# Kernel tuning notes

Hardware: AMD Instinct MI355X
Metric: run time of the kernel (lower is better)

Reference implementation:

```python
import jax, jax.numpy as jnp
import numpy as np

B, N, E, R, D, L = 2, 40000, 400000, 64, 64, 6
LN_EPS = 1e-5


def _layer_norm(x, g, b):
    mu = jnp.mean(x, axis=-1, keepdims=True)
    var = jnp.var(x, axis=-1, keepdims=True)
    return (x - mu) * jax.lax.rsqrt(var + LN_EPS) * g + b


def setup_inputs() -> dict:
    key = jax.random.key(0)
    ks = jax.random.split(key, 10)
    s = 0.05
    return {
        "rel_reps": jax.random.normal(ks[0], (B, R, D), jnp.float32),
        "h_index": jax.random.randint(ks[1], (B,), 0, N, jnp.int32),
        "r_index": jax.random.randint(ks[2], (B,), 0, R, jnp.int32),
        "edge_index": jax.random.randint(ks[3], (2, E), 0, N, jnp.int32),
        "edge_type": jax.random.randint(ks[4], (E,), 0, R, jnp.int32),
        "proj_w1": jax.random.normal(ks[5], (L, D, D), jnp.float32) * s,
        "proj_b1": jnp.zeros((L, D), jnp.float32),
        "proj_w2": jax.random.normal(ks[6], (L, D, D), jnp.float32) * s,
        "proj_b2": jnp.zeros((L, D), jnp.float32),
        "lin_w": jax.random.normal(ks[7], (L, 2 * D, D), jnp.float32) * s,
        "lin_b": jnp.zeros((L, D), jnp.float32),
        "ln_g": jnp.ones((L, D), jnp.float32),
        "ln_b": jnp.zeros((L, D), jnp.float32),
        "mlp_w": jax.random.normal(ks[8], (2 * D, 2 * D), jnp.float32) * s,
        "mlp_b": jnp.zeros((2 * D,), jnp.float32),
        "num_nodes": N,
    }


def reference(rel_reps, h_index, r_index, edge_index, edge_type,
              proj_w1, proj_b1, proj_w2, proj_b2,
              lin_w, lin_b, ln_g, ln_b, mlp_w, mlp_b, num_nodes):
    # EntityNBFNet.bellmanford with 6 GeneralizedRelationalConv layers
    # (distmult message, sum aggregate, layer_norm, relu, short_cut).
    batch = rel_reps.shape[0]
    query = rel_reps[jnp.arange(batch), r_index]                     # [B, D]
    boundary = jnp.zeros((batch, num_nodes, rel_reps.shape[-1]), rel_reps.dtype)
    boundary = boundary.at[jnp.arange(batch), h_index].set(query)    # [B, N, D]
    src, dst = edge_index[0], edge_index[1]

    def layer_step(x, params):
        pw1, pb1, pw2, pb2, lw, lb, lng, lnb = params
        # per-layer relation projection MLP (project_relations=True)
        rel = jax.nn.relu(jnp.einsum("brd,de->bre", rel_reps, pw1) + pb1)
        rel = jnp.einsum("brd,de->bre", rel, pw2) + pb2              # [B, R, D]
        # distmult message: x_src * rel_edge  -> [B, E, D]
        msg = jnp.take(x, src, axis=1) * jnp.take(rel, edge_type, axis=1)
        # sum aggregation (edge_weight = ones) + boundary self-message
        agg = jax.vmap(lambda m: jax.ops.segment_sum(m, dst, num_segments=num_nodes))(msg)
        agg = agg + boundary
        out = jnp.concatenate([x, agg], axis=-1) @ lw + lb           # [B, N, D]
        out = jax.nn.relu(_layer_norm(out, lng, lnb))
        out = out + x                                                # short cut
        return out, None

    x, _ = jax.lax.scan(layer_step, boundary,
                        (proj_w1, proj_b1, proj_w2, proj_b2, lin_w, lin_b, ln_g, ln_b))
    node_query = jnp.broadcast_to(query[:, None, :], x.shape)        # [B, N, D]
    feature = jnp.concatenate([x, node_query], axis=-1)              # [B, N, 2D]
    # embedd_out=True: MLP = Linear(2D, 2D) + ReLU
    embedd = jax.nn.relu(feature @ mlp_w + mlp_b)
    return embedd
```

## Files before the change

kernel.cpp:

```cpp
#include <hip/hip_runtime.h>
#include <hip/hip_bf16.h>

namespace {

constexpr int B = 2;
constexpr int N = 40000;
constexpr int E = 400000;
constexpr int R = 64;
constexpr int D = 64;
constexpr int L = 6;
constexpr float EPS = 1e-5f;
constexpr int NB = (N + 255) / 256;
constexpr int EB = (E + 255) / 256;

typedef _Float16 v8h __attribute__((ext_vector_type(8)));
typedef _Float16 v2h __attribute__((ext_vector_type(2)));
typedef float    v4f __attribute__((ext_vector_type(4)));

__device__ __forceinline__ unsigned int pack_h2(float a, float b) {
  v2h p; p.x = (_Float16)a; p.y = (_Float16)b;
  return __builtin_bit_cast(unsigned int, p);
}
__device__ __forceinline__ float2 unpack_h2(unsigned int u) {
  v2h p = __builtin_bit_cast(v2h, u);
  return make_float2((float)p.x, (float)p.y);
}


__global__ void k_init(const float* __restrict__ rel_reps,
                       const int* __restrict__ h_index, const int* __restrict__ r_index,
                       unsigned int* __restrict__ xb,
                       _Float16* __restrict__ xrow0, _Float16* __restrict__ xrow1,
                       float* __restrict__ query_f, _Float16* __restrict__ qh) {
  int d = threadIdx.x;
  int h0 = h_index[0], h1 = h_index[1];
  float q0 = rel_reps[r_index[0] * D + d];
  float q1 = rel_reps[(R + r_index[1]) * D + d];
  query_f[d * 2] = q0; query_f[d * 2 + 1] = q1;
  qh[d]     = (_Float16)q0;
  qh[D + d] = (_Float16)q1;
  if (h0 == h1) {
    xb[(size_t)h0 * D + d] = pack_h2(q0, q1);
  } else {
    xb[(size_t)h0 * D + d] = pack_h2(q0, 0.f);
    xb[(size_t)h1 * D + d] = pack_h2(0.f, q1);
  }
  xrow0[(size_t)h0 * 2 * D + d] = (_Float16)q0;
  xrow1[(size_t)h1 * 2 * D + d] = (_Float16)q1;
}

__global__ __launch_bounds__(64) void k_rel(
    const float* __restrict__ rel_reps,
    const float* __restrict__ pw1, const float* __restrict__ pb1,
    const float* __restrict__ pw2, const float* __restrict__ pb2,
    float* __restrict__ rel_f) {
  __shared__ float row[D];
  __shared__ float row2[D];
  int idx = blockIdx.x;
  int l = idx / (B * R);
  int br = idx - l * (B * R);
  int b = br / R, r = br - b * R;
  int d = threadIdx.x;
  row[d] = rel_reps[(size_t)br * D + d];
  __syncthreads();
  const float* w1 = pw1 + (size_t)l * D * D;
  float acc = pb1[l * D + d];
  for (int k = 0; k < D; ++k) acc = fmaf(row[k], w1[k * D + d], acc);
  row2[d] = fmaxf(acc, 0.f);
  __syncthreads();
  const float* w2 = pw2 + (size_t)l * D * D;
  float acc2 = pb2[l * D + d];
  for (int k = 0; k < D; ++k) acc2 = fmaf(row2[k], w2[k * D + d], acc2);
  rel_f[(((size_t)l * R + r) * D + d) * 2 + b] = acc2;
}

__global__ __launch_bounds__(256) void k_pack_rel(const float2* __restrict__ rel2,
                                                  unsigned int* __restrict__ rel_pk) {
  int i = blockIdx.x * 256 + threadIdx.x;
  if (i < L * R * D) {
    float2 v = rel2[i];
    rel_pk[i] = pack_h2(v.x, v.y);
  }
}

__global__ __launch_bounds__(64) void k_pack_w(const float* __restrict__ lin_w,
                                               unsigned short* __restrict__ Wf) {
  int idx = blockIdx.x;
  int l = idx >> 4;
  int ct = (idx >> 2) & 3, ks = idx & 3;
  int lane = threadIdx.x;
  int n = ct * 16 + (lane & 15);
  #pragma unroll
  for (int j = 0; j < 8; ++j) {
    int k = ks * 32 + (lane >> 4) * 8 + j;
    _Float16 v = (_Float16)lin_w[(size_t)l * 2 * D * D + (size_t)k * D + n];
    Wf[(size_t)l * 8192 + ((size_t)(ct * 4 + ks) * 64 + lane) * 8 + j] =
        __builtin_bit_cast(unsigned short, v);
  }
}

__global__ __launch_bounds__(64) void k_pack_wm(const float* __restrict__ mlp_w,
                                                unsigned short* __restrict__ Wm) {
  int idx = blockIdx.x;
  int ct = idx >> 2, ks = idx & 3;
  int lane = threadIdx.x;
  int n = ct * 16 + (lane & 15);
  #pragma unroll
  for (int j = 0; j < 8; ++j) {
    int k = ks * 32 + (lane >> 4) * 8 + j;
    _Float16 v = (_Float16)mlp_w[(size_t)k * 2 * D + n];
    Wm[((size_t)idx * 64 + lane) * 8 + j] = __builtin_bit_cast(unsigned short, v);
  }
}

__global__ __launch_bounds__(256) void k_hist(const int* __restrict__ dst,
                                              int* __restrict__ cnt) {
  int e = blockIdx.x * 256 + threadIdx.x;
  if (e < E) atomicAdd(&cnt[dst[e]], 1);
}

__global__ __launch_bounds__(256) void k_scan1(const int* __restrict__ cnt,
                                               int* __restrict__ row_ptr,
                                               int* __restrict__ bsum) {
  __shared__ int s[256];
  int t = threadIdx.x;
  int i = blockIdx.x * 256 + t;
  int v = (i < N) ? cnt[i] : 0;
  s[t] = v;
  __syncthreads();
  #pragma unroll
  for (int off = 1; off < 256; off <<= 1) {
    int u = (t >= off) ? s[t - off] : 0;
    __syncthreads();
    s[t] += u;
    __syncthreads();
  }
  if (i < N) row_ptr[i] = s[t] - v;
  if (t == 255) bsum[blockIdx.x] = s[255];
}

__global__ __launch_bounds__(256) void k_scan2(int* __restrict__ bsum,
                                               int* __restrict__ row_ptr) {
  __shared__ int s[NB];
  int t = threadIdx.x;
  if (t < NB) s[t] = bsum[t];
  __syncthreads();
  if (t == 0) {
    int run = 0;
    for (int i = 0; i < NB; ++i) { int v = s[i]; s[i] = run; run += v; }
    row_ptr[N] = run;
  }
  __syncthreads();
  if (t < NB) bsum[t] = s[t];
}

__global__ __launch_bounds__(256) void k_scan3(int* __restrict__ row_ptr,
                                               const int* __restrict__ bsum,
                                               int* __restrict__ cursor) {
  int i = blockIdx.x * 256 + threadIdx.x;
  if (i < N) {
    int v = row_ptr[i] + bsum[blockIdx.x];
    row_ptr[i] = v;
    cursor[i] = v;
  }
}

__global__ __launch_bounds__(256) void k_fill(const int* __restrict__ src,
                                              const int* __restrict__ dst,
                                              const int* __restrict__ etype,
                                              int* __restrict__ cursor,
                                              unsigned int* __restrict__ es) {
  int e = blockIdx.x * 256 + threadIdx.x;
  if (e < E) {
    int p = atomicAdd(&cursor[dst[e]], 1);
    es[p] = (unsigned int)src[e] | ((unsigned int)etype[e] << 16);
  }
}

__global__ __launch_bounds__(256, 8) void k_gather(
    const unsigned int* __restrict__ xb,
    _Float16* __restrict__ xrow0, _Float16* __restrict__ xrow1,
    const unsigned int* __restrict__ rel_pk,
    const int* __restrict__ row_ptr, const unsigned int* __restrict__ es,
    const float2* __restrict__ q2, const int* __restrict__ h_index, int first) {
  int tid = threadIdx.x;
  int lane = tid & 63;
  int n = (blockIdx.x * 256 + tid) >> 6;
  int h0 = h_index[0], h1 = h_index[1];
  int rs = row_ptr[n], re = row_ptr[n + 1];
  int m = min(re - rs, 64);
  unsigned int pkl = 0;
  if (lane < m) pkl = es[rs + lane];
  float a0 = 0.f, a1 = 0.f;
  if (first) {
    for (int j = 0; j < m; ++j) {
      unsigned int pk = __shfl(pkl, j);
      int s  = (int)(pk & 0xffffu);
      int et = (int)(pk >> 16);
      if (s == h0) { float2 xf = unpack_h2(xb[(size_t)s * D + lane]);
                     float2 rf = unpack_h2(rel_pk[et * D + lane]);
                     a0 = fmaf(xf.x, rf.x, a0); }
      if (s == h1) { float2 xf = unpack_h2(xb[(size_t)s * D + lane]);
                     float2 rf = unpack_h2(rel_pk[et * D + lane]);
                     a1 = fmaf(xf.y, rf.y, a1); }
    }
    for (int jj = rs + 64; jj < re; ++jj) {
      unsigned int pk = es[jj];
      int s  = (int)(pk & 0xffffu);
      int et = (int)(pk >> 16);
      if (s == h0) { float2 xf = unpack_h2(xb[(size_t)s * D + lane]);
                     float2 rf = unpack_h2(rel_pk[et * D + lane]);
                     a0 = fmaf(xf.x, rf.x, a0); }
      if (s == h1) { float2 xf = unpack_h2(xb[(size_t)s * D + lane]);
                     float2 rf = unpack_h2(rel_pk[et * D + lane]);
                     a1 = fmaf(xf.y, rf.y, a1); }
    }
  } else {
    int j = 0;
    for (; j + 4 <= m; j += 4) {
      unsigned int p0 = __shfl(pkl, j),     p1 = __shfl(pkl, j + 1);
      unsigned int p2 = __shfl(pkl, j + 2), p3 = __shfl(pkl, j + 3);
      unsigned int xa  = xb[(size_t)(p0 & 0xffffu) * D + lane];
      unsigned int xbv = xb[(size_t)(p1 & 0xffffu) * D + lane];
      unsigned int xc  = xb[(size_t)(p2 & 0xffffu) * D + lane];
      unsigned int xd  = xb[(size_t)(p3 & 0xffffu) * D + lane];
      unsigned int ra = rel_pk[(p0 >> 16) * D + lane];
      unsigned int rb = rel_pk[(p1 >> 16) * D + lane];
      unsigned int rc = rel_pk[(p2 >> 16) * D + lane];
      unsigned int rd = rel_pk[(p3 >> 16) * D + lane];
      float2 xf, rf;
      xf = unpack_h2(xa);  rf = unpack_h2(ra);
      a0 = fmaf(xf.x, rf.x, a0); a1 = fmaf(xf.y, rf.y, a1);
      xf = unpack_h2(xbv); rf = unpack_h2(rb);
      a0 = fmaf(xf.x, rf.x, a0); a1 = fmaf(xf.y, rf.y, a1);
      xf = unpack_h2(xc);  rf = unpack_h2(rc);
      a0 = fmaf(xf.x, rf.x, a0); a1 = fmaf(xf.y, rf.y, a1);
      xf = unpack_h2(xd);  rf = unpack_h2(rd);
      a0 = fmaf(xf.x, rf.x, a0); a1 = fmaf(xf.y, rf.y, a1);
    }
    for (; j < m; ++j) {
      unsigned int pk = __shfl(pkl, j);
      float2 xf = unpack_h2(xb[(size_t)(pk & 0xffffu) * D + lane]);
      float2 rf = unpack_h2(rel_pk[(pk >> 16) * D + lane]);
      a0 = fmaf(xf.x, rf.x, a0); a1 = fmaf(xf.y, rf.y, a1);
    }
    for (int jj = rs + 64; jj < re; ++jj) {
      unsigned int pk = es[jj];
      float2 xf = unpack_h2(xb[(size_t)(pk & 0xffffu) * D + lane]);
      float2 rf = unpack_h2(rel_pk[(pk >> 16) * D + lane]);
      a0 = fmaf(xf.x, rf.x, a0); a1 = fmaf(xf.y, rf.y, a1);
    }
  }
  if (n == h0) a0 += q2[lane].x;
  if (n == h1) a1 += q2[lane].y;
  xrow0[(size_t)n * 2 * D + D + lane] = (_Float16)a0;
  xrow1[(size_t)n * 2 * D + D + lane] = (_Float16)a1;
}

__global__ __launch_bounds__(64) void k_linear(
    unsigned int* __restrict__ xb,
    _Float16* __restrict__ xrow0, _Float16* __restrict__ xrow1,
    const unsigned short* __restrict__ Wf,
    const float* __restrict__ lin_b, const float* __restrict__ ln_g,
    const float* __restrict__ ln_b, int layer) {
  int lane = threadIdx.x;
  int nb = blockIdx.x * 16;
  int c = lane & 15, rg = lane >> 4;
  const v8h* wf = (const v8h*)(Wf + (size_t)layer * 8192);
  v8h Bf[4][4];
  #pragma unroll
  for (int ct = 0; ct < 4; ++ct)
    #pragma unroll
    for (int ks = 0; ks < 4; ++ks)
      Bf[ct][ks] = wf[(ct * 4 + ks) * 64 + lane];
  v4f acc0[4], acc1[4];
  #pragma unroll
  for (int ct = 0; ct < 4; ++ct) {
    acc0[ct] = (v4f){0.f, 0.f, 0.f, 0.f};
    acc1[ct] = (v4f){0.f, 0.f, 0.f, 0.f};
  }
  #pragma unroll
  for (int ks = 0; ks < 4; ++ks) {
    size_t aoff = (size_t)(nb + c) * 2 * D + ks * 32 + rg * 8;
    v8h A0 = *(const v8h*)(xrow0 + aoff);
    v8h A1 = *(const v8h*)(xrow1 + aoff);
    #pragma unroll
    for (int ct = 0; ct < 4; ++ct) {
      acc0[ct] = __builtin_amdgcn_mfma_f32_16x16x32_f16(A0, Bf[ct][ks], acc0[ct], 0, 0, 0);
      acc1[ct] = __builtin_amdgcn_mfma_f32_16x16x32_f16(A1, Bf[ct][ks], acc1[ct], 0, 0, 0);
    }
  }
  float bias4[4], g4[4], be4[4];
  #pragma unroll
  for (int ct = 0; ct < 4; ++ct) {
    int d = ct * 16 + c;
    bias4[ct] = lin_b[layer * D + d];
    g4[ct]    = ln_g[layer * D + d];
    be4[ct]   = ln_b[layer * D + d];
  }
  #pragma unroll
  for (int j = 0; j < 4; ++j) {
    int node = nb + rg * 4 + j;
    float v0[4], v1[4];
    float s10 = 0.f, s20 = 0.f, s11 = 0.f, s21 = 0.f;
    #pragma unroll
    for (int ct = 0; ct < 4; ++ct) {
      v0[ct] = acc0[ct][j] + bias4[ct];
      v1[ct] = acc1[ct][j] + bias4[ct];
      s10 += v0[ct]; s20 += v0[ct] * v0[ct];
      s11 += v1[ct]; s21 += v1[ct] * v1[ct];
    }
    #pragma unroll
    for (int mk = 1; mk < 16; mk <<= 1) {
      s10 += __shfl_xor(s10, mk); s20 += __shfl_xor(s20, mk);
      s11 += __shfl_xor(s11, mk); s21 += __shfl_xor(s21, mk);
    }
    float mu0 = s10 * (1.f / D), var0 = s20 * (1.f / D) - mu0 * mu0;
    float mu1 = s11 * (1.f / D), var1 = s21 * (1.f / D) - mu1 * mu1;
    float rs0 = rsqrtf(var0 + EPS), rs1 = rsqrtf(var1 + EPS);
    #pragma unroll
    for (int ct = 0; ct < 4; ++ct) {
      int d = ct * 16 + c;
      float o0 = fmaxf((v0[ct] - mu0) * rs0 * g4[ct] + be4[ct], 0.f);
      float o1 = fmaxf((v1[ct] - mu1) * rs1 * g4[ct] + be4[ct], 0.f);
      float2 xv = unpack_h2(xb[(size_t)node * D + d]);
      float r0 = o0 + xv.x, r1 = o1 + xv.y;
      xb[(size_t)node * D + d] = pack_h2(r0, r1);
      xrow0[(size_t)node * 2 * D + d] = (_Float16)r0;
      xrow1[(size_t)node * 2 * D + d] = (_Float16)r1;
    }
  }
}

__global__ __launch_bounds__(64) void k_mlp(
    const _Float16* __restrict__ xrow0, const _Float16* __restrict__ xrow1,
    const _Float16* __restrict__ qh,
    const unsigned short* __restrict__ Wm,
    const float* __restrict__ mlp_b,
    float* __restrict__ outf) {
  int lane = threadIdx.x;
  int nb = blockIdx.x * 16;
  int c = lane & 15, rg = lane >> 4;
  const v8h* wm = (const v8h*)Wm;
  v4f acc0[8], acc1[8];
  #pragma unroll
  for (int ct = 0; ct < 8; ++ct) {
    acc0[ct] = (v4f){0.f, 0.f, 0.f, 0.f};
    acc1[ct] = (v4f){0.f, 0.f, 0.f, 0.f};
  }
  #pragma unroll
  for (int ks = 0; ks < 4; ++ks) {
    v8h A0, A1;
    if (ks < 2) {
      size_t aoff = (size_t)(nb + c) * 2 * D + ks * 32 + rg * 8;
      A0 = *(const v8h*)(xrow0 + aoff);
      A1 = *(const v8h*)(xrow1 + aoff);
    } else {
      int qoff = (ks - 2) * 32 + rg * 8;
      A0 = *(const v8h*)(qh + qoff);
      A1 = *(const v8h*)(qh + D + qoff);
    }
    #pragma unroll
    for (int ct = 0; ct < 8; ++ct) {
      v8h Bv = wm[(ct * 4 + ks) * 64 + lane];
      acc0[ct] = __builtin_amdgcn_mfma_f32_16x16x32_f16(A0, Bv, acc0[ct], 0, 0, 0);
      acc1[ct] = __builtin_amdgcn_mfma_f32_16x16x32_f16(A1, Bv, acc1[ct], 0, 0, 0);
    }
  }
  #pragma unroll
  for (int ct = 0; ct < 8; ++ct) {
    int d = ct * 16 + c;
    float bias = mlp_b[d];
    #pragma unroll
    for (int j = 0; j < 4; ++j) {
      int node = nb + rg * 4 + j;
      outf[(size_t)node * 2 * D + d]       = fmaxf(acc0[ct][j] + bias, 0.f);
      outf[((size_t)N + node) * 2 * D + d] = fmaxf(acc1[ct][j] + bias, 0.f);
    }
  }
}

}

extern "C" void kernel_launch(void* const* d_in, const int* in_sizes, int n_in,
                              void* d_out, int out_size, void* d_ws, size_t ws_size,
                              hipStream_t stream) {
  const float* rel_reps = (const float*)d_in[0];
  const int* h_index    = (const int*)d_in[1];
  const int* r_index    = (const int*)d_in[2];
  const int* edge_index = (const int*)d_in[3];
  const int* edge_type  = (const int*)d_in[4];
  const float* proj_w1  = (const float*)d_in[5];
  const float* proj_b1  = (const float*)d_in[6];
  const float* proj_w2  = (const float*)d_in[7];
  const float* proj_b2  = (const float*)d_in[8];
  const float* lin_w    = (const float*)d_in[9];
  const float* lin_b    = (const float*)d_in[10];
  const float* ln_g     = (const float*)d_in[11];
  const float* ln_b     = (const float*)d_in[12];
  const float* mlp_w    = (const float*)d_in[13];
  const float* mlp_b    = (const float*)d_in[14];

  float* rel_all = (float*)d_ws;
  float* query   = rel_all + (size_t)2 * L * R * D;
  int*   cnt     = (int*)(query + 2 * D);
  int*   row_ptr = cnt + N;
  int*   cursor  = row_ptr + (N + 1);
  unsigned int* es  = (unsigned int*)(cursor + N);
  int*   bsum    = (int*)(es + E);
  unsigned int* xb = (unsigned int*)(bsum + NB);
  unsigned int* rel_pk = xb + (size_t)N * D;
  unsigned short* Wf = (unsigned short*)(rel_pk + (size_t)L * R * D);
  _Float16* xrow0 = (_Float16*)(Wf + (size_t)L * 8192);
  _Float16* xrow1 = xrow0 + (size_t)N * 2 * D;
  unsigned short* Wm = (unsigned short*)(xrow1 + (size_t)N * 2 * D);
  _Float16* qh = (_Float16*)(Wm + 16384);

  const int* srcp = edge_index;
  const int* dstp = edge_index + E;

  hipMemsetAsync(xb, 0, (size_t)N * D * sizeof(unsigned int), stream);
  hipMemsetAsync(xrow0, 0, (size_t)N * 2 * D * sizeof(_Float16) * 2, stream);
  hipMemsetAsync(cnt, 0, N * sizeof(int), stream);
  k_init<<<1, 64, 0, stream>>>(rel_reps, h_index, r_index,
                               xb, xrow0, xrow1, query, qh);
  k_rel<<<L * B * R, 64, 0, stream>>>(rel_reps, proj_w1, proj_b1, proj_w2, proj_b2, rel_all);
  k_pack_rel<<<(L * R * D + 255) / 256, 256, 0, stream>>>((const float2*)rel_all, rel_pk);
  k_pack_w<<<L * 16, 64, 0, stream>>>(lin_w, Wf);
  k_pack_wm<<<32, 64, 0, stream>>>(mlp_w, Wm);
  k_hist<<<EB, 256, 0, stream>>>(dstp, cnt);
  k_scan1<<<NB, 256, 0, stream>>>(cnt, row_ptr, bsum);
  k_scan2<<<1, 256, 0, stream>>>(bsum, row_ptr);
  k_scan3<<<NB, 256, 0, stream>>>(row_ptr, bsum, cursor);
  k_fill<<<EB, 256, 0, stream>>>(srcp, dstp, edge_type, cursor, es);

  for (int l = 0; l < L; ++l) {
    k_gather<<<N / 4, 256, 0, stream>>>(xb, xrow0, xrow1,
                                        rel_pk + (size_t)l * R * D,
                                        row_ptr, es, (const float2*)query, h_index,
                                        (l == 0) ? 1 : 0);
    k_linear<<<N / 16, 64, 0, stream>>>(xb, xrow0, xrow1,
                                        Wf, lin_b, ln_g, ln_b, l);
  }
  k_mlp<<<N / 16, 64, 0, stream>>>(xrow0, xrow1, qh, Wm, mlp_b, (float*)d_out);
}
```

Measured before the change: 393.5 us.

## Process two destination nodes per wavefront in gather with 8-byte loads

The gather kernel now splits each 64-lane wavefront into two 32-lane halves, each handling its own destination node and loading two packed feature pairs per lane with 8-byte loads. This halves the grid and is meant to raise memory-level parallelism and cut wasted lanes for low-degree nodes, since the average in-degree is about 10. In exchange the two halves run in lockstep up to the larger degree of the pair, and the neighbour buffer shrinks from 64 to 32 entries, so more edges take the slower serial tail loop.

```diff
diff --git a/kernel.cpp b/kernel.cpp
--- a/kernel.cpp
+++ b/kernel.cpp
@@ -185,76 +185,111 @@
     const float2* __restrict__ q2, const int* __restrict__ h_index, int first) {
   int tid = threadIdx.x;
   int lane = tid & 63;
-  int n = (blockIdx.x * 256 + tid) >> 6;
+  int h = lane >> 5;
+  int ln = lane & 31;
+  int w = (blockIdx.x * 256 + tid) >> 6;
+  int n = w * 2 + h;
   int h0 = h_index[0], h1 = h_index[1];
-  int rs = row_ptr[n], re = row_ptr[n + 1];
-  int m = min(re - rs, 64);
-  unsigned int pkl = 0;
-  if (lane < m) pkl = es[rs + lane];
-  float a0 = 0.f, a1 = 0.f;
+  int rp = 0;
+  if (lane < 3) rp = row_ptr[2 * w + lane];
+  int rs = __shfl(rp, h);
+  int re = __shfl(rp, h + 1);
+  int deg = re - rs;
+  int dc = min(deg, 32);
+  unsigned int esv = 0;
+  if (ln < dc) esv = es[rs + ln];
+  float a0x = 0.f, a0y = 0.f, a1x = 0.f, a1y = 0.f;
   if (first) {
-    for (int j = 0; j < m; ++j) {
-      unsigned int pk = __shfl(pkl, j);
-      int s  = (int)(pk & 0xffffu);
-      int et = (int)(pk >> 16);
-      if (s == h0) { float2 xf = unpack_h2(xb[(size_t)s * D + lane]);
-                     float2 rf = unpack_h2(rel_pk[et * D + lane]);
-                     a0 = fmaf(xf.x, rf.x, a0); }
-      if (s == h1) { float2 xf = unpack_h2(xb[(size_t)s * D + lane]);
-                     float2 rf = unpack_h2(rel_pk[et * D + lane]);
-                     a1 = fmaf(xf.y, rf.y, a1); }
-    }
-    for (int jj = rs + 64; jj < re; ++jj) {
-      unsigned int pk = es[jj];
-      int s  = (int)(pk & 0xffffu);
-      int et = (int)(pk >> 16);
-      if (s == h0) { float2 xf = unpack_h2(xb[(size_t)s * D + lane]);
-                     float2 rf = unpack_h2(rel_pk[et * D + lane]);
-                     a0 = fmaf(xf.x, rf.x, a0); }
-      if (s == h1) { float2 xf = unpack_h2(xb[(size_t)s * D + lane]);
-                     float2 rf = unpack_h2(rel_pk[et * D + lane]);
-                     a1 = fmaf(xf.y, rf.y, a1); }
+    for (int j = 0; j < dc; ++j) {
+      unsigned int pk = __shfl(esv, (h << 5) | j);
+      int s = (int)(pk & 0xffffu), et = (int)(pk >> 16);
+      if (s == h0 || s == h1) {
+        uint2 xv = *(const uint2*)&xb[(size_t)s * D + 2 * ln];
+        uint2 rv = *(const uint2*)&rel_pk[et * D + 2 * ln];
+        float2 xfx = unpack_h2(xv.x), xfy = unpack_h2(xv.y);
+        float2 rfx = unpack_h2(rv.x), rfy = unpack_h2(rv.y);
+        if (s == h0) { a0x = fmaf(xfx.x, rfx.x, a0x); a0y = fmaf(xfy.x, rfy.x, a0y); }
+        if (s == h1) { a1x = fmaf(xfx.y, rfx.y, a1x); a1y = fmaf(xfy.y, rfy.y, a1y); }
+      }
+    }
+    for (int j = rs + 32; j < re; ++j) {
+      unsigned int pk = es[j];
+      int s = (int)(pk & 0xffffu), et = (int)(pk >> 16);
+      if (s == h0 || s == h1) {
+        uint2 xv = *(const uint2*)&xb[(size_t)s * D + 2 * ln];
+        uint2 rv = *(const uint2*)&rel_pk[et * D + 2 * ln];
+        float2 xfx = unpack_h2(xv.x), xfy = unpack_h2(xv.y);
+        float2 rfx = unpack_h2(rv.x), rfy = unpack_h2(rv.y);
+        if (s == h0) { a0x = fmaf(xfx.x, rfx.x, a0x); a0y = fmaf(xfy.x, rfy.x, a0y); }
+        if (s == h1) { a1x = fmaf(xfx.y, rfx.y, a1x); a1y = fmaf(xfy.y, rfy.y, a1y); }
+      }
     }
   } else {
-    int j = 0;
-    for (; j + 4 <= m; j += 4) {
-      unsigned int p0 = __shfl(pkl, j),     p1 = __shfl(pkl, j + 1);
-      unsigned int p2 = __shfl(pkl, j + 2), p3 = __shfl(pkl, j + 3);
-      unsigned int xa  = xb[(size_t)(p0 & 0xffffu) * D + lane];
-      unsigned int xbv = xb[(size_t)(p1 & 0xffffu) * D + lane];
-      unsigned int xc  = xb[(size_t)(p2 & 0xffffu) * D + lane];
-      unsigned int xd  = xb[(size_t)(p3 & 0xffffu) * D + lane];
-      unsigned int ra = rel_pk[(p0 >> 16) * D + lane];
-      unsigned int rb = rel_pk[(p1 >> 16) * D + lane];
-      unsigned int rc = rel_pk[(p2 >> 16) * D + lane];
-      unsigned int rd = rel_pk[(p3 >> 16) * D + lane];
-      float2 xf, rf;
-      xf = unpack_h2(xa);  rf = unpack_h2(ra);
-      a0 = fmaf(xf.x, rf.x, a0); a1 = fmaf(xf.y, rf.y, a1);
-      xf = unpack_h2(xbv); rf = unpack_h2(rb);
-      a0 = fmaf(xf.x, rf.x, a0); a1 = fmaf(xf.y, rf.y, a1);
-      xf = unpack_h2(xc);  rf = unpack_h2(rc);
-      a0 = fmaf(xf.x, rf.x, a0); a1 = fmaf(xf.y, rf.y, a1);
-      xf = unpack_h2(xd);  rf = unpack_h2(rd);
-      a0 = fmaf(xf.x, rf.x, a0); a1 = fmaf(xf.y, rf.y, a1);
-    }
-    for (; j < m; ++j) {
-      unsigned int pk = __shfl(pkl, j);
-      float2 xf = unpack_h2(xb[(size_t)(pk & 0xffffu) * D + lane]);
-      float2 rf = unpack_h2(rel_pk[(pk >> 16) * D + lane]);
-      a0 = fmaf(xf.x, rf.x, a0); a1 = fmaf(xf.y, rf.y, a1);
-    }
-    for (int jj = rs + 64; jj < re; ++jj) {
-      unsigned int pk = es[jj];
-      float2 xf = unpack_h2(xb[(size_t)(pk & 0xffffu) * D + lane]);
-      float2 rf = unpack_h2(rel_pk[(pk >> 16) * D + lane]);
-      a0 = fmaf(xf.x, rf.x, a0); a1 = fmaf(xf.y, rf.y, a1);
-    }
-  }
-  if (n == h0) a0 += q2[lane].x;
-  if (n == h1) a1 += q2[lane].y;
-  xrow0[(size_t)n * 2 * D + D + lane] = (_Float16)a0;
-  xrow1[(size_t)n * 2 * D + D + lane] = (_Float16)a1;
+    int rounds = (dc + 3) >> 2;
+    int maxr = max(__shfl(rounds, 0), __shfl(rounds, 32));
+    for (int jr = 0; jr < maxr; ++jr) {
+      int j = jr * 4;
+      int i0 = max(min(j + 0, dc - 1), 0), i1 = max(min(j + 1, dc - 1), 0);
+      int i2 = max(min(j + 2, dc - 1), 0), i3 = max(min(j + 3, dc - 1), 0);
+      unsigned int p0 = __shfl(esv, (h << 5) | i0);
+      unsigned int p1 = __shfl(esv, (h << 5) | i1);
+      unsigned int p2 = __shfl(esv, (h << 5) | i2);
+      unsigned int p3 = __shfl(esv, (h << 5) | i3);
+      uint2 xv0 = *(const uint2*)&xb[(size_t)(p0 & 0xffffu) * D + 2 * ln];
+      uint2 xv1 = *(const uint2*)&xb[(size_t)(p1 & 0xffffu) * D + 2 * ln];
+      uint2 xv2 = *(const uint2*)&xb[(size_t)(p2 & 0xffffu) * D + 2 * ln];
+      uint2 xv3 = *(const uint2*)&xb[(size_t)(p3 & 0xffffu) * D + 2 * ln];
+      uint2 rv0 = *(const uint2*)&rel_pk[(p0 >> 16) * D + 2 * ln];
+      uint2 rv1 = *(const uint2*)&rel_pk[(p1 >> 16) * D + 2 * ln];
+      uint2 rv2 = *(const uint2*)&rel_pk[(p2 >> 16) * D + 2 * ln];
+      uint2 rv3 = *(const uint2*)&rel_pk[(p3 >> 16) * D + 2 * ln];
+      if (j + 0 < dc) {
+        float2 xfx = unpack_h2(xv0.x), xfy = unpack_h2(xv0.y);
+        float2 rfx = unpack_h2(rv0.x), rfy = unpack_h2(rv0.y);
+        a0x = fmaf(xfx.x, rfx.x, a0x); a1x = fmaf(xfx.y, rfx.y, a1x);
+        a0y = fmaf(xfy.x, rfy.x, a0y); a1y = fmaf(xfy.y, rfy.y, a1y);
+      }
+      if (j + 1 < dc) {
+        float2 xfx = unpack_h2(xv1.x), xfy = unpack_h2(xv1.y);
+        float2 rfx = unpack_h2(rv1.x), rfy = unpack_h2(rv1.y);
+        a0x = fmaf(xfx.x, rfx.x, a0x); a1x = fmaf(xfx.y, rfx.y, a1x);
+        a0y = fmaf(xfy.x, rfy.x, a0y); a1y = fmaf(xfy.y, rfy.y, a1y);
+      }
+      if (j + 2 < dc) {
+        float2 xfx = unpack_h2(xv2.x), xfy = unpack_h2(xv2.y);
+        float2 rfx = unpack_h2(rv2.x), rfy = unpack_h2(rv2.y);
+        a0x = fmaf(xfx.x, rfx.x, a0x); a1x = fmaf(xfx.y, rfx.y, a1x);
+        a0y = fmaf(xfy.x, rfy.x, a0y); a1y = fmaf(xfy.y, rfy.y, a1y);
+      }
+      if (j + 3 < dc) {
+        float2 xfx = unpack_h2(xv3.x), xfy = unpack_h2(xv3.y);
+        float2 rfx = unpack_h2(rv3.x), rfy = unpack_h2(rv3.y);
+        a0x = fmaf(xfx.x, rfx.x, a0x); a1x = fmaf(xfx.y, rfx.y, a1x);
+        a0y = fmaf(xfy.x, rfy.x, a0y); a1y = fmaf(xfy.y, rfy.y, a1y);
+      }
+    }
+    for (int j = rs + 32; j < re; ++j) {
+      unsigned int pk = es[j];
+      uint2 xv = *(const uint2*)&xb[(size_t)(pk & 0xffffu) * D + 2 * ln];
+      uint2 rv = *(const uint2*)&rel_pk[(pk >> 16) * D + 2 * ln];
+      float2 xfx = unpack_h2(xv.x), xfy = unpack_h2(xv.y);
+      float2 rfx = unpack_h2(rv.x), rfy = unpack_h2(rv.y);
+      a0x = fmaf(xfx.x, rfx.x, a0x); a1x = fmaf(xfx.y, rfx.y, a1x);
+      a0y = fmaf(xfy.x, rfy.x, a0y); a1y = fmaf(xfy.y, rfy.y, a1y);
+    }
+  }
+  if (n == h0) {
+    float4 qq = *(const float4*)&q2[2 * ln];
+    a0x += qq.x; a0y += qq.z;
+  }
+  if (n == h1) {
+    float4 qq = *(const float4*)&q2[2 * ln];
+    a1x += qq.y; a1y += qq.w;
+  }
+  v2h s0; s0.x = (_Float16)a0x; s0.y = (_Float16)a0y;
+  v2h s1; s1.x = (_Float16)a1x; s1.y = (_Float16)a1y;
+  *(v2h*)&xrow0[(size_t)n * 2 * D + D + 2 * ln] = s0;
+  *(v2h*)&xrow1[(size_t)n * 2 * D + D + 2 * ln] = s1;
 }
 
 __global__ __launch_bounds__(64) void k_linear(
@@ -435,7 +470,7 @@
   k_fill<<<EB, 256, 0, stream>>>(srcp, dstp, edge_type, cursor, es);
 
   for (int l = 0; l < L; ++l) {
-    k_gather<<<N / 4, 256, 0, stream>>>(xb, xrow0, xrow1,
+    k_gather<<<N / 8, 256, 0, stream>>>(xb, xrow0, xrow1,
                                         rel_pk + (size_t)l * R * D,
                                         row_ptr, es, (const float2*)query, h_index,
                                         (l == 0) ? 1 : 0);
```

New measurement: 376.3 us. -4.4%, faster.
